# Optimization experiments

Hardware: AMD Instinct MI355X
Metric: run time of the kernel (lower is better)

The kernel has to match this reference:

```python
import jax, jax.numpy as jnp
import numpy as np
import math

FACTOR = 5


def _prob_attention(queries, keys, values, index_sample):
    # queries/keys/values: [B, H, L, D]; index_sample: [L_Q, sample_k] int
    B, H, L_Q, D = queries.shape
    L_K = keys.shape[2]
    u = min(FACTOR * int(math.ceil(math.log(L_Q))), L_Q)  # n_top queries

    # --- _prob_QK: random-sampled scores, heuristic M, top-u query selection ---
    # gather sampled keys per query position: [B, H, L_Q, sample_k, D]
    K_sample = keys[:, :, index_sample, :]
    Q_K_sample = jnp.einsum('bhqd,bhqkd->bhqk', queries, K_sample)  # [B,H,L_Q,sample_k]
    M = Q_K_sample.max(axis=-1) - Q_K_sample.sum(axis=-1) / L_K      # [B,H,L_Q]
    M_top = jax.lax.top_k(M, u)[1]                                   # [B,H,u] indices

    # gather the selected queries and compute full scores against all keys
    Q_reduce = jnp.take_along_axis(queries, M_top[..., None], axis=2)  # [B,H,u,D]
    scores = jnp.einsum('bhud,bhkd->bhuk', Q_reduce, keys)             # [B,H,u,L_K]

    # scale: original does `scale = self.scale or 1/sqrt(D)`; with scale=True this
    # multiplies by True (i.e. *1), so scores are left unscaled -- faithful.

    # --- causal ProbMask: triu(1) rows gathered at the selected query indices ---
    causal = jnp.triu(jnp.ones((L_Q, L_K), dtype=bool), 1)  # [L_Q, L_K]
    row_mask = causal[M_top]                                 # [B,H,u,L_K]
    scores = jnp.where(row_mask, -jnp.inf, scores)

    attn = jax.nn.softmax(scores, axis=-1)                   # [B,H,u,L_K]

    # --- initial context (mask_flag=True): cumulative sum of V over time ---
    context = jnp.cumsum(values, axis=2)                     # [B,H,L_Q,D]

    # --- scatter-update context at selected query positions ---
    upd = jnp.einsum('bhuk,bhkd->bhud', attn, values)        # [B,H,u,D]
    b_idx = jnp.arange(B)[:, None, None]
    h_idx = jnp.arange(H)[None, :, None]
    context = context.at[b_idx, h_idx, M_top].set(upd)

    return jnp.transpose(context, (0, 2, 1, 3))              # [B,L_Q,H,D]


def setup_inputs() -> dict:
    key = jax.random.key(0)
    kq, kk, kv, ki = jax.random.split(key, 4)
    B, H, L, D = 4, 8, 2048, 64
    sample_k = FACTOR * int(math.ceil(math.log(L)))  # 40
    queries = jax.random.normal(kq, (B, H, L, D), dtype=jnp.float32)
    keys = jax.random.normal(kk, (B, H, L, D), dtype=jnp.float32)
    values = jax.random.normal(kv, (B, H, L, D), dtype=jnp.float32)
    index_sample = jax.random.randint(ki, (L, sample_k), 0, L)
    return {"queries": queries, "keys": keys, "values": values,
            "index_sample": index_sample}


def reference(queries, keys, values, index_sample):
    return _prob_attention(queries, keys, values, index_sample)
```

## Files before the change

kernel.cpp:

```cpp
#include <hip/hip_runtime.h>
#include <math.h>

#define B_ 4
#define H_ 8
#define L_ 2048
#define D_ 64
#define SK_ 40
#define U_ 40
#define CK 256
#define NCHUNK (L_ / CK)
#define QG 8
#define NQG (U_ / QG)
#define CSB 32

__global__ __launch_bounds__(1024) void k_mcs(
    const float* __restrict__ Q, const float* __restrict__ K,
    const int* __restrict__ idxs, const float* __restrict__ V,
    float* __restrict__ M, float* __restrict__ out) {
  if (blockIdx.x < CSB) {
    __shared__ float segtot[16][64];
    int bh = blockIdx.x;
    int b = bh >> 3, h = bh & 7;
    int t = threadIdx.x;
    int seg = t >> 6, d = t & 63;
    const float* Vb = V + (size_t)bh * L_ * D_;
    int base = seg * 128;
    float s = 0.f;
    for (int l = 0; l < 128; ++l) s += Vb[(size_t)(base + l) * D_ + d];
    segtot[seg][d] = s;
    __syncthreads();
    float run = 0.f;
    for (int ss = 0; ss < seg; ++ss) run += segtot[ss][d];
    for (int l = 0; l < 128; ++l) {
      int gl = base + l;
      run += Vb[(size_t)gl * D_ + d];
      out[(((size_t)b * L_ + gl) * H_ + h) * D_ + d] = run;
    }
    return;
  }

  int blk = blockIdx.x - CSB;
  int x = blk & 7;
  int j = blk >> 3;
  int bh = ((j >> 7) << 3) | x;
  int qc = j & 127;
  int wave = threadIdx.x >> 6;
  int lane = threadIdx.x & 63;
  int q = qc * 16 + wave;

  int g  = lane >> 3;
  int li = lane & 7;

  const float4* qrow = (const float4*)(Q + ((size_t)bh * L_ + q) * D_);
  float4 qa = qrow[li], qb = qrow[li + 8];
  int myidx = (lane < SK_) ? idxs[q * SK_ + lane] : 0;
  const float* Kb = K + (size_t)bh * L_ * D_;

  int kis[5];
#pragma unroll
  for (int t = 0; t < 5; ++t) kis[t] = __shfl(myidx, t * 8 + g, 64);

  float4 ka[5], kb[5];
#pragma unroll
  for (int t = 0; t < 5; ++t) {
    const float4* kr = (const float4*)(Kb + (size_t)kis[t] * D_);
    ka[t] = kr[li];
    kb[t] = kr[li + 8];
  }

  float d[5];
#pragma unroll
  for (int t = 0; t < 5; ++t) {
    d[t] = qa.x * ka[t].x + qa.y * ka[t].y + qa.z * ka[t].z + qa.w * ka[t].w
         + qb.x * kb[t].x + qb.y * kb[t].y + qb.z * kb[t].z + qb.w * kb[t].w;
  }
  float mx = -INFINITY, sm = 0.f;
#pragma unroll
  for (int t = 0; t < 5; ++t) {
    float v = d[t];
    v += __shfl_xor(v, 1, 64);
    v += __shfl_xor(v, 2, 64);
    v += __shfl_xor(v, 4, 64);
    mx = fmaxf(mx, v);
    sm += v;
  }
  mx = fmaxf(mx, __shfl_xor(mx, 8, 64));
  mx = fmaxf(mx, __shfl_xor(mx, 16, 64));
  mx = fmaxf(mx, __shfl_xor(mx, 32, 64));
  sm += __shfl_xor(sm, 8, 64);
  sm += __shfl_xor(sm, 16, 64);
  sm += __shfl_xor(sm, 32, 64);
  if (lane == 0) M[bh * L_ + q] = mx - sm * (1.0f / (float)L_);
}

__global__ __launch_bounds__(1024) void k_topk(
    const float* __restrict__ M, int* __restrict__ Mtop) {
  __shared__ unsigned keys[L_];
  __shared__ int hist[256];
  __shared__ int Gs[256];
  __shared__ unsigned ctl_prefix;
  __shared__ int ctl_need, ctl_cnt, ctl_min;
  __shared__ int wmin[16];
  int bh = blockIdx.x;
  int tid = threadIdx.x;

  for (int i = tid; i < L_; i += 1024) {
    unsigned u = __float_as_uint(M[bh * L_ + i]);
    keys[i] = (u & 0x80000000u) ? ~u : (u | 0x80000000u);
  }
  if (tid == 0) { ctl_prefix = 0u; ctl_need = U_; ctl_cnt = 0; }
  __syncthreads();

  unsigned prefix = 0u, pmask = 0u;
#pragma unroll
  for (int pass = 0; pass < 4; ++pass) {
    int shift = 24 - 8 * pass;
    if (tid < 256) hist[tid] = 0;
    __syncthreads();
    for (int i = tid; i < L_; i += 1024) {
      unsigned k = keys[i];
      if ((k & pmask) == prefix) atomicAdd(&hist[(k >> shift) & 0xffu], 1);
    }
    __syncthreads();
    if (tid < 64) {
      int b0 = tid * 4;
      int h0 = hist[b0], h1 = hist[b0 + 1], h2 = hist[b0 + 2], h3 = hist[b0 + 3];
      int gs = h0 + h1 + h2 + h3;
      int S = gs;
#pragma unroll
      for (int d = 1; d < 64; d <<= 1) {
        int v = __shfl_down(S, d, 64);
        if (tid + d < 64) S += v;
      }
      int E = S - gs;
      Gs[b0 + 3] = E;
      Gs[b0 + 2] = E + h3;
      Gs[b0 + 1] = E + h3 + h2;
      Gs[b0 + 0] = E + h3 + h2 + h1;
    }
    __syncthreads();
    int need = ctl_need;
    if (tid < 256) {
      int G = Gs[tid], h = hist[tid];
      if (G < need && need <= G + h) {
        ctl_prefix = prefix | ((unsigned)tid << shift);
        ctl_need = need - G;
      }
    }
    __syncthreads();
    prefix = ctl_prefix;
    pmask |= (0xffu << shift);
  }

  unsigned v40 = prefix;
  int tiesNeeded = ctl_need;
  __syncthreads();

  for (int i = tid; i < L_; i += 1024) {
    if (keys[i] > v40) {
      int slot = atomicAdd(&ctl_cnt, 1);
      Mtop[bh * U_ + slot] = i;
    }
  }
  __syncthreads();
  int base = ctl_cnt;
  int last = -1;
  for (int t = 0; t < tiesNeeded; ++t) {
    int lmin = 0x7fffffff;
    for (int i = tid; i < L_; i += 1024)
      if (keys[i] == v40 && i > last) lmin = min(lmin, i);
#pragma unroll
    for (int d = 32; d > 0; d >>= 1) lmin = min(lmin, __shfl_xor(lmin, d, 64));
    if ((tid & 63) == 0) wmin[tid >> 6] = lmin;
    __syncthreads();
    if (tid == 0) {
      int m = wmin[0];
      for (int w = 1; w < 16; ++w) m = min(m, wmin[w]);
      Mtop[bh * U_ + base + t] = m;
      ctl_min = m;
    }
    __syncthreads();
    last = ctl_min;
  }
}

__global__ __launch_bounds__(256) void k_attn_part(
    const float* __restrict__ Q, const float* __restrict__ K,
    const float* __restrict__ V, const int* __restrict__ Mtop,
    float* __restrict__ pm, float* __restrict__ ps, float* __restrict__ pacc) {
  int blk = blockIdx.x;
  int x = blk & 7;
  int j = blk >> 3;
  int bh = (j / 40) * 8 + x;
  int rem = j % 40;
  int c  = rem / NQG;
  int qg = rem % NQG;

  int tid = threadIdx.x;
  int w = tid >> 6, lane = tid & 63;
  __shared__ float Qs[QG][D_];
  __shared__ float P[QG][CK];
  __shared__ float pvred[4][QG][D_];
  __shared__ int q0s[QG];
  if (tid < QG) q0s[tid] = Mtop[bh * U_ + qg * QG + tid];
  __syncthreads();
  for (int i = tid; i < QG * D_; i += 256) {
    int u = i >> 6, d = i & 63;
    Qs[u][d] = Q[((size_t)bh * L_ + q0s[u]) * D_ + d];
  }
  __syncthreads();

  int kg = c * CK + tid;
  const float4* kr = (const float4*)(K + ((size_t)bh * L_ + kg) * D_);
  float4 kv[16];
#pragma unroll
  for (int j4 = 0; j4 < 16; ++j4) kv[j4] = kr[j4];
#pragma unroll
  for (int u = 0; u < QG; ++u) {
    float acc = 0.f;
#pragma unroll
    for (int j4 = 0; j4 < 16; ++j4) {
      float4 qv = *(const float4*)&Qs[u][j4 * 4];
      acc += qv.x * kv[j4].x + qv.y * kv[j4].y + qv.z * kv[j4].z + qv.w * kv[j4].w;
    }
    P[u][tid] = (kg <= q0s[u]) ? acc : -INFINITY;
  }
  __syncthreads();

#pragma unroll
  for (int uu = 0; uu < 2; ++uu) {
    int u = w * 2 + uu;
    float v0 = P[u][lane], v1 = P[u][lane + 64];
    float v2 = P[u][lane + 128], v3 = P[u][lane + 192];
    float m = fmaxf(fmaxf(v0, v1), fmaxf(v2, v3));
    for (int o = 32; o > 0; o >>= 1) m = fmaxf(m, __shfl_xor(m, o, 64));
    float e0 = (v0 == -INFINITY) ? 0.f : expf(v0 - m);
    float e1 = (v1 == -INFINITY) ? 0.f : expf(v1 - m);
    float e2 = (v2 == -INFINITY) ? 0.f : expf(v2 - m);
    float e3 = (v3 == -INFINITY) ? 0.f : expf(v3 - m);
    float s = e0 + e1 + e2 + e3;
    for (int o = 32; o > 0; o >>= 1) s += __shfl_xor(s, o, 64);
    P[u][lane] = e0; P[u][lane + 64] = e1;
    P[u][lane + 128] = e2; P[u][lane + 192] = e3;
    if (lane == 0) {
      int p = (bh * NCHUNK + c) * U_ + qg * QG + u;
      pm[p] = m; ps[p] = s;
    }
  }
  __syncthreads();

  const float* Vb = V + ((size_t)bh * L_ + c * CK + w * 64) * D_;
  float acc[QG];
#pragma unroll
  for (int u = 0; u < QG; ++u) acc[u] = 0.f;
  for (int k4 = 0; k4 < 16; ++k4) {
    float4 pv[QG];
#pragma unroll
    for (int u = 0; u < QG; ++u) pv[u] = *(const float4*)&P[u][w * 64 + k4 * 4];
    float va = Vb[(size_t)(k4 * 4 + 0) * D_ + lane];
    float vb = Vb[(size_t)(k4 * 4 + 1) * D_ + lane];
    float vc = Vb[(size_t)(k4 * 4 + 2) * D_ + lane];
    float vd = Vb[(size_t)(k4 * 4 + 3) * D_ + lane];
#pragma unroll
    for (int u = 0; u < QG; ++u)
      acc[u] += pv[u].x * va + pv[u].y * vb + pv[u].z * vc + pv[u].w * vd;
  }
#pragma unroll
  for (int u = 0; u < QG; ++u) pvred[w][u][lane] = acc[u];
  __syncthreads();
#pragma unroll
  for (int uu = 0; uu < 2; ++uu) {
    int u = w * 2 + uu;
    float tot = pvred[0][u][lane] + pvred[1][u][lane] +
                pvred[2][u][lane] + pvred[3][u][lane];
    int p = (bh * NCHUNK + c) * U_ + qg * QG + u;
    pacc[(size_t)p * 64 + lane] = tot;
  }
}

__global__ __launch_bounds__(256) void k_attn_reduce(
    const float* __restrict__ pm, const float* __restrict__ ps,
    const float* __restrict__ pacc, const int* __restrict__ Mtop,
    float* __restrict__ out) {
  int g = blockIdx.x * 4 + (threadIdx.x >> 6);
  int lane = threadIdx.x & 63;
  int bh = g / U_, u = g % U_;
  int b = bh >> 3, h = bh & 7;
  int q0 = Mtop[bh * U_ + u];
  float pmv[NCHUNK];
  float M = -INFINITY;
#pragma unroll
  for (int c = 0; c < NCHUNK; ++c) {
    pmv[c] = pm[(bh * NCHUNK + c) * U_ + u];
    M = fmaxf(M, pmv[c]);
  }
  float T = 0.f, o = 0.f;
#pragma unroll
  for (int c = 0; c < NCHUNK; ++c) {
    float wgt = (pmv[c] == -INFINITY) ? 0.f : expf(pmv[c] - M);
    T += ps[(bh * NCHUNK + c) * U_ + u] * wgt;
    o += pacc[((size_t)(bh * NCHUNK + c) * U_ + u) * 64 + lane] * wgt;
  }
  out[(((size_t)b * L_ + q0) * H_ + h) * D_ + lane] = o / T;
}

extern "C" void kernel_launch(void* const* d_in, const int* in_sizes, int n_in,
                              void* d_out, int out_size, void* d_ws, size_t ws_size,
                              hipStream_t stream) {
  const float* Q = (const float*)d_in[0];
  const float* K = (const float*)d_in[1];
  const float* V = (const float*)d_in[2];
  const int* idxs = (const int*)d_in[3];
  float* out = (float*)d_out;

  char* ws = (char*)d_ws;
  float* M      = (float*)(ws + 0);
  int*   Mtop   = (int*)(ws + 262144);
  float* pm     = (float*)(ws + 270336);
  float* ps     = (float*)(ws + 311296);
  float* pacc   = (float*)(ws + 352256);

  k_mcs<<<CSB + (B_ * H_ * L_) / 16, 1024, 0, stream>>>(Q, K, idxs, V, M, out);
  k_topk<<<B_ * H_, 1024, 0, stream>>>(M, Mtop);
  k_attn_part<<<B_ * H_ * NCHUNK * NQG, 256, 0, stream>>>(Q, K, V, Mtop, pm, ps, pacc);
  k_attn_reduce<<<(B_ * H_ * U_) / 4, 256, 0, stream>>>(pm, ps, pacc, Mtop, out);
}
```

Measured before the change: 69.18 us.

## Split V cumsum into segment-sum and scan phases across two kernels

The causal cumsum of V was a serial 128-step scan per thread in 32 blocks inside the first kernel, producing both segment totals and the output. It now computes 64-row segment sums in the first kernel, writes them to workspace, and performs the prefix scan and output write in 256 extra blocks prepended to the attention-partial kernel. This spreads the scan across more blocks and overlaps it with attention work, at the cost of an extra workspace round trip and redundant prefix summation per segment. Correctness relies on the reduce kernel overwriting the selected rows after the scan blocks have written them.

Measured after the change: 69.33 us. About the same (+0.2%).

```diff
diff --git a/kernel.cpp b/kernel.cpp
--- a/kernel.cpp
+++ b/kernel.cpp
@@ -12,29 +12,26 @@
 #define QG 8
 #define NQG (U_ / QG)
 #define CSB 32
+#define SEG 64
+#define NSEGS (L_ / SEG)
+#define CSB2 256
 
 __global__ __launch_bounds__(1024) void k_mcs(
     const float* __restrict__ Q, const float* __restrict__ K,
     const int* __restrict__ idxs, const float* __restrict__ V,
-    float* __restrict__ M, float* __restrict__ out) {
+    float* __restrict__ M, float* __restrict__ segsum) {
   if (blockIdx.x < CSB) {
-    __shared__ float segtot[16][64];
     int bh = blockIdx.x;
-    int b = bh >> 3, h = bh & 7;
-    int t = threadIdx.x;
-    int seg = t >> 6, d = t & 63;
+    int wv = threadIdx.x >> 6;
+    int lane = threadIdx.x & 63;
     const float* Vb = V + (size_t)bh * L_ * D_;
-    int base = seg * 128;
-    float s = 0.f;
-    for (int l = 0; l < 128; ++l) s += Vb[(size_t)(base + l) * D_ + d];
-    segtot[seg][d] = s;
-    __syncthreads();
-    float run = 0.f;
-    for (int ss = 0; ss < seg; ++ss) run += segtot[ss][d];
-    for (int l = 0; l < 128; ++l) {
-      int gl = base + l;
-      run += Vb[(size_t)gl * D_ + d];
-      out[(((size_t)b * L_ + gl) * H_ + h) * D_ + d] = run;
+#pragma unroll
+    for (int si = 0; si < 2; ++si) {
+      int seg = wv * 2 + si;
+      int base = seg * SEG;
+      float s = 0.f;
+      for (int l = 0; l < SEG; ++l) s += Vb[(size_t)(base + l) * D_ + lane];
+      segsum[((size_t)bh * NSEGS + seg) * D_ + lane] = s;
     }
     return;
   }
@@ -187,8 +184,30 @@
 __global__ __launch_bounds__(256) void k_attn_part(
     const float* __restrict__ Q, const float* __restrict__ K,
     const float* __restrict__ V, const int* __restrict__ Mtop,
-    float* __restrict__ pm, float* __restrict__ ps, float* __restrict__ pacc) {
-  int blk = blockIdx.x;
+    const float* __restrict__ segsum,
+    float* __restrict__ pm, float* __restrict__ ps, float* __restrict__ pacc,
+    float* __restrict__ out) {
+  if (blockIdx.x < CSB2) {
+    int bid = blockIdx.x;
+    int bh = bid >> 3, o = bid & 7;
+    int b = bh >> 3, h = bh & 7;
+    int wv = threadIdx.x >> 6;
+    int lane = threadIdx.x & 63;
+    int seg = o * 4 + wv;
+    float run = 0.f;
+    for (int s2 = 0; s2 < seg; ++s2)
+      run += segsum[((size_t)bh * NSEGS + s2) * D_ + lane];
+    const float* Vb = V + (size_t)bh * L_ * D_;
+    int base = seg * SEG;
+    for (int l = 0; l < SEG; ++l) {
+      int gl = base + l;
+      run += Vb[(size_t)gl * D_ + lane];
+      out[(((size_t)b * L_ + gl) * H_ + h) * D_ + lane] = run;
+    }
+    return;
+  }
+
+  int blk = blockIdx.x - CSB2;
   int x = blk & 7;
   int j = blk >> 3;
   int bh = (j / 40) * 8 + x;
@@ -315,13 +334,15 @@
 
   char* ws = (char*)d_ws;
   float* M      = (float*)(ws + 0);
-  int*   Mtop   = (int*)(ws + 262144);
-  float* pm     = (float*)(ws + 270336);
-  float* ps     = (float*)(ws + 311296);
-  float* pacc   = (float*)(ws + 352256);
-
-  k_mcs<<<CSB + (B_ * H_ * L_) / 16, 1024, 0, stream>>>(Q, K, idxs, V, M, out);
+  float* segsum = (float*)(ws + 262144);
+  int*   Mtop   = (int*)(ws + 524288);
+  float* pm     = (float*)(ws + 532480);
+  float* ps     = (float*)(ws + 573440);
+  float* pacc   = (float*)(ws + 614400);
+
+  k_mcs<<<CSB + (B_ * H_ * L_) / 16, 1024, 0, stream>>>(Q, K, idxs, V, M, segsum);
   k_topk<<<B_ * H_, 1024, 0, stream>>>(M, Mtop);
-  k_attn_part<<<B_ * H_ * NCHUNK * NQG, 256, 0, stream>>>(Q, K, V, Mtop, pm, ps, pacc);
+  k_attn_part<<<CSB2 + B_ * H_ * NCHUNK * NQG, 256, 0, stream>>>(
+      Q, K, V, Mtop, segsum, pm, ps, pacc, out);
   k_attn_reduce<<<(B_ * H_ * U_) / 4, 256, 0, stream>>>(pm, ps, pacc, Mtop, out);
 }
```

## Split V cumsum into segment-prefix pass and parallel write pass alongside top-k

Applied to the files above, without the earlier changes.

The serial per-(b,h) cumulative sum of V, done by only 32 blocks each walking 128 rows per thread, is split into two passes. The first pass, still inside k_mcs, computes per-16-row segment prefix totals into a new workspace buffer. The second pass is folded into the k_topk launch as 256 extra blocks that each expand 16 segments into the full cumsum output, running alongside the top-k blocks. This shortens the serial chain and spreads output writes over more blocks, at the cost of an extra prefix buffer and a second read of V.

Result: no change. 68.47 us (median of 2 runs) (-1.0%).

```diff
diff --git a/kernel.cpp b/kernel.cpp
--- a/kernel.cpp
+++ b/kernel.cpp
@@ -12,30 +12,39 @@
 #define QG 8
 #define NQG (U_ / QG)
 #define CSB 32
+#define SEG2 16
+#define NSEG2 (L_ / SEG2)
+#define PB 256
 
 __global__ __launch_bounds__(1024) void k_mcs(
     const float* __restrict__ Q, const float* __restrict__ K,
     const int* __restrict__ idxs, const float* __restrict__ V,
-    float* __restrict__ M, float* __restrict__ out) {
+    float* __restrict__ M, float* __restrict__ pfx) {
   if (blockIdx.x < CSB) {
-    __shared__ float segtot[16][64];
+    __shared__ float wt[16][64];
     int bh = blockIdx.x;
-    int b = bh >> 3, h = bh & 7;
-    int t = threadIdx.x;
-    int seg = t >> 6, d = t & 63;
+    int w = threadIdx.x >> 6, lane = threadIdx.x & 63;
     const float* Vb = V + (size_t)bh * L_ * D_;
-    int base = seg * 128;
-    float s = 0.f;
-    for (int l = 0; l < 128; ++l) s += Vb[(size_t)(base + l) * D_ + d];
-    segtot[seg][d] = s;
-    __syncthreads();
-    float run = 0.f;
-    for (int ss = 0; ss < seg; ++ss) run += segtot[ss][d];
-    for (int l = 0; l < 128; ++l) {
-      int gl = base + l;
-      run += Vb[(size_t)gl * D_ + d];
-      out[(((size_t)b * L_ + gl) * H_ + h) * D_ + d] = run;
-    }
+    float pres[8];
+    float pre = 0.f;
+#pragma unroll
+    for (int i = 0; i < 8; ++i) {
+      int base = w * 128 + i * SEG2;
+      float s = 0.f;
+      for (int l = 0; l < SEG2; ++l) s += Vb[(size_t)(base + l) * D_ + lane];
+      pres[i] = pre;
+      pre += s;
+    }
+    wt[w][lane] = pre;
+    __syncthreads();
+    float base = 0.f;
+    for (int ww = 0; ww < 16; ++ww) {
+      float v = wt[ww][lane];
+      if (ww < w) base += v;
+    }
+#pragma unroll
+    for (int i = 0; i < 8; ++i)
+      pfx[((size_t)bh * NSEG2 + w * 8 + i) * D_ + lane] = base + pres[i];
     return;
   }
 
@@ -94,7 +103,26 @@
 }
 
 __global__ __launch_bounds__(1024) void k_topk(
-    const float* __restrict__ M, int* __restrict__ Mtop) {
+    const float* __restrict__ M, const float* __restrict__ V,
+    const float* __restrict__ pfx, int* __restrict__ Mtop,
+    float* __restrict__ out) {
+  if (blockIdx.x >= CSB) {
+    int bid = blockIdx.x - CSB;
+    int bh = bid >> 3, oct = bid & 7;
+    int b = bh >> 3, h = bh & 7;
+    int w = threadIdx.x >> 6, lane = threadIdx.x & 63;
+    int seg = oct * 16 + w;
+    float run = pfx[((size_t)bh * NSEG2 + seg) * D_ + lane];
+    const float* Vb = V + (size_t)bh * L_ * D_;
+    int base = seg * SEG2;
+    for (int l = 0; l < SEG2; ++l) {
+      int gl = base + l;
+      run += Vb[(size_t)gl * D_ + lane];
+      out[(((size_t)b * L_ + gl) * H_ + h) * D_ + lane] = run;
+    }
+    return;
+  }
+
   __shared__ unsigned keys[L_];
   __shared__ int hist[256];
   __shared__ int Gs[256];
@@ -314,14 +342,15 @@
   float* out = (float*)d_out;
 
   char* ws = (char*)d_ws;
-  float* M      = (float*)(ws + 0);
-  int*   Mtop   = (int*)(ws + 262144);
-  float* pm     = (float*)(ws + 270336);
-  float* ps     = (float*)(ws + 311296);
-  float* pacc   = (float*)(ws + 352256);
-
-  k_mcs<<<CSB + (B_ * H_ * L_) / 16, 1024, 0, stream>>>(Q, K, idxs, V, M, out);
-  k_topk<<<B_ * H_, 1024, 0, stream>>>(M, Mtop);
+  float* M    = (float*)(ws + 0);
+  float* pfx  = (float*)(ws + 262144);
+  int*   Mtop = (int*)(ws + 1310720);
+  float* pm   = (float*)(ws + 1318912);
+  float* ps   = (float*)(ws + 1359872);
+  float* pacc = (float*)(ws + 1400832);
+
+  k_mcs<<<CSB + (B_ * H_ * L_) / 16, 1024, 0, stream>>>(Q, K, idxs, V, M, pfx);
+  k_topk<<<CSB + PB, 1024, 0, stream>>>(M, V, pfx, Mtop, out);
   k_attn_part<<<B_ * H_ * NCHUNK * NQG, 256, 0, stream>>>(Q, K, V, Mtop, pm, ps, pacc);
   k_attn_reduce<<<(B_ * H_ * U_) / 4, 256, 0, stream>>>(pm, ps, pacc, Mtop, out);
 }
```
